# Performance work log

Hardware: AMD Instinct MI355X
Metric: run time of the kernel (lower is better)

## Reference

```python
import jax, jax.numpy as jnp
import numpy as np

B, T, E, H = 2, 2048, 1024, 16
Dh = E // H  # head_size = 64


def setup_inputs() -> dict:
    key = jax.random.key(0)
    ks = jax.random.split(key, 6)
    s = E ** -0.5
    x = jax.random.normal(ks[0], (B, T, E), dtype=jnp.float32)
    Wq = jax.random.normal(ks[1], (H, E, Dh), dtype=jnp.float32) * s
    Wk = jax.random.normal(ks[2], (H, E, Dh), dtype=jnp.float32) * s
    Wv = jax.random.normal(ks[3], (H, E, Dh), dtype=jnp.float32) * s
    wo_w = jax.random.normal(ks[4], (E, E), dtype=jnp.float32) * s  # torch Linear weight [out,in]
    wo_b = jax.random.normal(ks[5], (E,), dtype=jnp.float32) * 0.01
    return {"x": x, "Wq": Wq, "Wk": Wk, "Wv": Wv, "wo_w": wo_w, "wo_b": wo_b}


def reference(x, Wq, Wk, Wv, wo_w, wo_b):
    # Batched equivalent of the per-head Python loop: project all heads at once.
    q = jnp.einsum('bte,hed->bhtd', x, Wq)
    k = jnp.einsum('bte,hed->bhtd', x, Wk)
    v = jnp.einsum('bte,hed->bhtd', x, Wv)
    scale = Dh ** -0.5
    scores = jnp.einsum('bhtd,bhsd->bhts', q, k) * scale  # [B,H,T,T]
    causal = jnp.tril(jnp.ones((T, T), dtype=bool))
    scores = jnp.where(causal, scores, jnp.finfo(scores.dtype).min)
    att = jax.nn.softmax(scores, axis=-1)
    out = jnp.einsum('bhts,bhsd->bhtd', att, v)  # [B,H,T,Dh]
    # concat heads (head order along last dim, matching torch.cat over heads)
    out = out.transpose(0, 2, 1, 3).reshape(B, T, E)
    return out @ wo_w.T + wo_b
```

## Files before the change

### kernel.cpp

```cpp
#include <hip/hip_runtime.h>

#define B_ 2
#define T_ 2048
#define E_ 1024
#define H_ 16
#define DH 64

typedef unsigned short u16;
typedef unsigned int u32;
typedef __bf16 bf16x8 __attribute__((ext_vector_type(8)));
typedef float f32x4 __attribute__((ext_vector_type(4)));

__device__ __forceinline__ u16 f2bf(float f) {
  u32 u = __builtin_bit_cast(u32, f);
  u = u + 0x7FFFu + ((u >> 16) & 1u);
  return (u16)(u >> 16);
}
__device__ __forceinline__ float bf2f(u16 v) {
  return __builtin_bit_cast(float, (u32)v << 16);
}
__device__ __forceinline__ bf16x8 ldfrag(const u16* p) { return *(const bf16x8*)p; }

__device__ __forceinline__ void gload_lds16(const u16* g, u16* l) {
  __builtin_amdgcn_global_load_lds((const __attribute__((address_space(1))) u32*)g,
                                   (__attribute__((address_space(3))) u32*)l, 16, 0, 0);
}
template <int IMM>
__device__ __forceinline__ float swz(float v) {
  return __builtin_bit_cast(float, __builtin_amdgcn_ds_swizzle(__builtin_bit_cast(int, v), IMM));
}

__global__ void k_conv_x(const float* __restrict__ src, u16* __restrict__ dst) {
  u32 i = (blockIdx.x * 256u + threadIdx.x) * 8u;
  float4 a = *(const float4*)(src + i);
  float4 b = *(const float4*)(src + i + 4);
  uint4 v;
  v.x = (u32)f2bf(a.x) | ((u32)f2bf(a.y) << 16);
  v.y = (u32)f2bf(a.z) | ((u32)f2bf(a.w) << 16);
  v.z = (u32)f2bf(b.x) | ((u32)f2bf(b.y) << 16);
  v.w = (u32)f2bf(b.z) | ((u32)f2bf(b.w) << 16);
  *(uint4*)(dst + i) = v;
}

__global__ __launch_bounds__(256) void k_conv_wT(const float* __restrict__ Wq, const float* __restrict__ Wk,
                                                 const float* __restrict__ Wv, u16* __restrict__ wT) {
  __shared__ __align__(16) u16 Ls[64][68];
  const int t = threadIdx.x;
  const int e0 = blockIdx.x * 64;
  const int h = blockIdx.y;
  const int which = blockIdx.z;
  const float* src = (which == 0) ? Wq : ((which == 1) ? Wk : Wv);
  const float scale = (which == 0) ? 0.18033688011112042f : 1.0f;
#pragma unroll
  for (int p = 0; p < 4; p++) {
    int idx = p * 256 + t;
    int row = idx >> 4, ch = idx & 15;
    float4 v = *(const float4*)(src + ((size_t)h * E_ + e0 + row) * DH + ch * 4);
    uint2 pk;
    pk.x = (u32)f2bf(v.x * scale) | ((u32)f2bf(v.y * scale) << 16);
    pk.y = (u32)f2bf(v.z * scale) | ((u32)f2bf(v.w * scale) << 16);
    *(uint2*)(&Ls[row][ch * 4]) = pk;
  }
  __syncthreads();
  u16* dst = wT + ((size_t)which * H_ + h) * (DH * E_);
#pragma unroll
  for (int p = 0; p < 4; p++) {
    int idx = p * 256 + t;
    int d = idx >> 4, ec = idx & 15;
    uint2 pk;
    pk.x = (u32)Ls[ec * 4 + 0][d] | ((u32)Ls[ec * 4 + 1][d] << 16);
    pk.y = (u32)Ls[ec * 4 + 2][d] | ((u32)Ls[ec * 4 + 3][d] << 16);
    *(uint2*)(dst + (size_t)d * E_ + e0 + ec * 4) = pk;
  }
}

__global__ __launch_bounds__(256, 3) void k_qkv(const u16* __restrict__ xb, const u16* __restrict__ wT,
                                                u16* __restrict__ Qb, u16* __restrict__ Kb,
                                                u16* __restrict__ VbT) {
  __shared__ __align__(16) u16 As[128 * 64];
  __shared__ __align__(16) u16 Bs[128 * 64];
  const int tid = threadIdx.x;
  const int w = tid >> 6, lane = tid & 63, quad = lane >> 4, lr = lane & 15;
  const int wr = w >> 1, wc = w & 1;
  const int t0 = blockIdx.x * 128;
  const int n0 = blockIdx.y * 128;
  const int sr = lane >> 3, sc = lane & 7;

  f32x4 acc[4][4];
  const f32x4 z4 = {0.f, 0.f, 0.f, 0.f};
#pragma unroll
  for (int i = 0; i < 4; i++)
#pragma unroll
    for (int j = 0; j < 4; j++) acc[i][j] = z4;

  for (int k0 = 0; k0 < E_; k0 += 64) {
    __syncthreads();
#pragma unroll
    for (int ii = 0; ii < 4; ii++) {
      int ra = w * 32 + ii * 8 + sr;
      gload_lds16(xb + (size_t)(t0 + ra) * E_ + k0 + ((sc ^ (ra & 7)) << 3),
                  As + (w * 32 + ii * 8) * 64);
      gload_lds16(wT + (size_t)(n0 + ra) * E_ + k0 + ((sc ^ (ra & 7)) << 3),
                  Bs + (w * 32 + ii * 8) * 64);
    }
    __syncthreads();
#pragma unroll
    for (int kk = 0; kk < 2; kk++) {
      bf16x8 af[4], bfv[4];
#pragma unroll
      for (int rt = 0; rt < 4; rt++) {
        int row = wr * 64 + rt * 16 + lr;
        af[rt] = ldfrag(As + row * 64 + (((kk * 4 + quad) ^ (row & 7)) << 3));
      }
#pragma unroll
      for (int ct = 0; ct < 4; ct++) {
        int row = wc * 64 + ct * 16 + lr;
        bfv[ct] = ldfrag(Bs + row * 64 + (((kk * 4 + quad) ^ (row & 7)) << 3));
      }
#pragma unroll
      for (int rt = 0; rt < 4; rt++)
#pragma unroll
        for (int ct = 0; ct < 4; ct++)
          acc[rt][ct] = __builtin_amdgcn_mfma_f32_16x16x32_bf16(af[rt], bfv[ct], acc[rt][ct], 0, 0, 0);
    }
  }

  const int qkv = n0 >> 10;
  if (qkv < 2) {
    u16* outp = (qkv == 0) ? Qb : Kb;
#pragma unroll
    for (int rt = 0; rt < 4; rt++)
#pragma unroll
      for (int ct = 0; ct < 4; ct++) {
        int n = n0 + wc * 64 + ct * 16 + lr;
        int h = (n >> 6) & 15, d = n & 63;
#pragma unroll
        for (int r = 0; r < 4; r++) {
          int t = t0 + wr * 64 + rt * 16 + quad * 4 + r;
          int bb = t >> 11, tt = t & 2047;
          outp[(((size_t)bb * H_ + h) * T_ + tt) * DH + d] = f2bf(acc[rt][ct][r]);
        }
      }
  } else {
#pragma unroll
    for (int rt = 0; rt < 4; rt++)
#pragma unroll
      for (int ct = 0; ct < 4; ct++) {
        int n = n0 + wc * 64 + ct * 16 + lr;
        int h = (n >> 6) & 15, d = n & 63;
        int t = t0 + wr * 64 + rt * 16 + quad * 4;
        int bb = t >> 11, tt = t & 2047;
        uint2 pk;
        pk.x = (u32)f2bf(acc[rt][ct][0]) | ((u32)f2bf(acc[rt][ct][1]) << 16);
        pk.y = (u32)f2bf(acc[rt][ct][2]) | ((u32)f2bf(acc[rt][ct][3]) << 16);
        *(uint2*)(VbT + (((size_t)bb * H_ + h) * DH + d) * T_ + tt) = pk;
      }
  }
}

__global__ __launch_bounds__(256, 4) void k_attn(const u16* __restrict__ Qb, const u16* __restrict__ Kb,
                                                 const u16* __restrict__ VbT, u16* __restrict__ O0,
                                                 u16* __restrict__ O1, float* __restrict__ Mb,
                                                 float* __restrict__ Lb) {
  __shared__ __align__(16) u16 Qs[64][72];
  __shared__ __align__(16) u16 Ks[64][72];
  __shared__ __align__(16) u16 Vts[64][72];
  __shared__ __align__(16) u16 Ps[64][72];
  const int tid = threadIdx.x;
  const int w = tid >> 6, lane = tid & 63, quad = lane >> 4, lr = lane & 15;
  const int i = blockIdx.x >> 1, s = blockIdx.x & 1;
  const int h = blockIdx.y, bb = blockIdx.z;
  const u16* qb = Qb + ((size_t)bb * H_ + h) * (size_t)(T_ * DH);
  const u16* kb = Kb + ((size_t)bb * H_ + h) * (size_t)(T_ * DH);
  const u16* vbT = VbT + ((size_t)bb * H_ + h) * (size_t)(T_ * DH);
  const f32x4 z4 = {0.f, 0.f, 0.f, 0.f};

  for (int jb = 0; jb < 2; jb++) {
    const int qt = jb ? i : (31 - i);
    const int sg = jb ? (1 - s) : s;
    const int t0 = qt * 64;
    __syncthreads();
#pragma unroll
    for (int p = 0; p < 2; p++) {
      int lin = p * 256 + tid;
      int r = lin >> 3, c = (lin & 7) * 8;
      *(uint4*)(&Qs[r][c]) = *(const uint4*)(qb + (size_t)(t0 + r) * DH + c);
    }

    f32x4 o_acc[4];
#pragma unroll
    for (int ct = 0; ct < 4; ct++) o_acc[ct] = z4;
    float m_i[4], l_i[4];
#pragma unroll
    for (int r = 0; r < 4; r++) { m_i[r] = -__builtin_inff(); l_i[r] = 0.f; }

    for (int jt = sg; jt <= qt; jt += 2) {
      const int j0 = jt * 64;
      __syncthreads();
#pragma unroll
      for (int p = 0; p < 2; p++) {
        int lin = p * 256 + tid;
        int r = lin >> 3, c = (lin & 7) * 8;
        *(uint4*)(&Ks[r][c]) = *(const uint4*)(kb + (size_t)(j0 + r) * DH + c);
        *(uint4*)(&Vts[r][c]) = *(const uint4*)(vbT + (size_t)r * T_ + j0 + c);
      }
      __syncthreads();

      f32x4 s_acc[4];
#pragma unroll
      for (int ct = 0; ct < 4; ct++) s_acc[ct] = z4;
      bf16x8 aq0 = ldfrag(&Qs[w * 16 + lr][quad * 8]);
      bf16x8 aq1 = ldfrag(&Qs[w * 16 + lr][32 + quad * 8]);
#pragma unroll
      for (int ct = 0; ct < 4; ct++) {
        bf16x8 b0 = ldfrag(&Ks[ct * 16 + lr][quad * 8]);
        bf16x8 b1 = ldfrag(&Ks[ct * 16 + lr][32 + quad * 8]);
        s_acc[ct] = __builtin_amdgcn_mfma_f32_16x16x32_bf16(aq0, b0, s_acc[ct], 0, 0, 0);
        s_acc[ct] = __builtin_amdgcn_mfma_f32_16x16x32_bf16(aq1, b1, s_acc[ct], 0, 0, 0);
      }

      if (jt == qt) {
        int trow = w * 16 + quad * 4;
#pragma unroll
        for (int ct = 0; ct < 4; ct++) {
          int sc = ct * 16 + lr;
#pragma unroll
          for (int r = 0; r < 4; r++)
            if (sc > trow + r) s_acc[ct][r] = -__builtin_inff();
        }
      }

      float alpha[4], rsum[4];
#pragma unroll
      for (int r = 0; r < 4; r++) {
        float v = fmaxf(fmaxf(s_acc[0][r], s_acc[1][r]), fmaxf(s_acc[2][r], s_acc[3][r]));
        v = fmaxf(v, swz<0x041F>(v));
        v = fmaxf(v, swz<0x081F>(v));
        v = fmaxf(v, swz<0x101F>(v));
        v = fmaxf(v, swz<0x201F>(v));
        float mnew = fmaxf(m_i[r], v);
        alpha[r] = __builtin_amdgcn_exp2f(m_i[r] - mnew);
        m_i[r] = mnew;
        rsum[r] = 0.f;
      }
#pragma unroll
      for (int ct = 0; ct < 4; ct++)
#pragma unroll
        for (int r = 0; r < 4; r++) {
          float p = __builtin_amdgcn_exp2f(s_acc[ct][r] - m_i[r]);
          rsum[r] += p;
          Ps[w * 16 + quad * 4 + r][ct * 16 + lr] = (u16)(__builtin_bit_cast(u32, p) >> 16);
        }
#pragma unroll
      for (int r = 0; r < 4; r++) {
        float v = rsum[r];
        v += swz<0x041F>(v);
        v += swz<0x081F>(v);
        v += swz<0x101F>(v);
        v += swz<0x201F>(v);
        l_i[r] = l_i[r] * alpha[r] + v;
      }
#pragma unroll
      for (int ct = 0; ct < 4; ct++)
#pragma unroll
        for (int r = 0; r < 4; r++) o_acc[ct][r] *= alpha[r];

      bf16x8 ap0 = ldfrag(&Ps[w * 16 + lr][quad * 8]);
      bf16x8 ap1 = ldfrag(&Ps[w * 16 + lr][32 + quad * 8]);
#pragma unroll
      for (int ct = 0; ct < 4; ct++) {
        bf16x8 b0 = ldfrag(&Vts[ct * 16 + lr][quad * 8]);
        bf16x8 b1 = ldfrag(&Vts[ct * 16 + lr][32 + quad * 8]);
        o_acc[ct] = __builtin_amdgcn_mfma_f32_16x16x32_bf16(ap0, b0, o_acc[ct], 0, 0, 0);
        o_acc[ct] = __builtin_amdgcn_mfma_f32_16x16x32_bf16(ap1, b1, o_acc[ct], 0, 0, 0);
      }
    }

    u16* op = (sg == 0) ? O0 : O1;
    float inv[4];
#pragma unroll
    for (int r = 0; r < 4; r++) inv[r] = (l_i[r] > 0.f) ? (1.0f / l_i[r]) : 0.f;
#pragma unroll
    for (int ct = 0; ct < 4; ct++)
#pragma unroll
      for (int r = 0; r < 4; r++) {
        int t = t0 + w * 16 + quad * 4 + r;
        op[((size_t)bb * T_ + t) * E_ + h * DH + ct * 16 + lr] = f2bf(o_acc[ct][r] * inv[r]);
      }
    if (lr == 0) {
#pragma unroll
      for (int r = 0; r < 4; r++) {
        int t = t0 + w * 16 + quad * 4 + r;
        int idx = ((sg * B_ + bb) * H_ + h) * T_ + t;
        Mb[idx] = m_i[r];
        Lb[idx] = l_i[r];
      }
    }
  }
}

__global__ void k_combine(u16* __restrict__ AO, const u16* __restrict__ O1,
                          const float* __restrict__ Mb, const float* __restrict__ Lb) {
  int idx = blockIdx.x * 256 + threadIdx.x;
  int e0 = idx * 4;
  int bb = e0 >> 21, t = (e0 >> 10) & 2047, hh = (e0 >> 6) & 15;
  int r0 = (bb * H_ + hh) * T_ + t;
  int r1 = r0 + B_ * H_ * T_;
  float m0 = Mb[r0], l0 = Lb[r0], m1 = Mb[r1], l1 = Lb[r1];
  float m = fmaxf(m0, m1);
  float w0 = l0 * __builtin_amdgcn_exp2f(m0 - m);
  float w1 = l1 * __builtin_amdgcn_exp2f(m1 - m);
  float inv = 1.0f / (w0 + w1);
  float a0 = w0 * inv, a1 = w1 * inv;
  uint2 u0 = *(const uint2*)(AO + e0);
  uint2 u1 = *(const uint2*)(O1 + e0);
  float f0 = a0 * bf2f((u16)u0.x) + a1 * bf2f((u16)u1.x);
  float f1 = a0 * bf2f((u16)(u0.x >> 16)) + a1 * bf2f((u16)(u1.x >> 16));
  float f2 = a0 * bf2f((u16)u0.y) + a1 * bf2f((u16)u1.y);
  float f3 = a0 * bf2f((u16)(u0.y >> 16)) + a1 * bf2f((u16)(u1.y >> 16));
  uint2 o;
  o.x = (u32)f2bf(f0) | ((u32)f2bf(f1) << 16);
  o.y = (u32)f2bf(f2) | ((u32)f2bf(f3) << 16);
  *(uint2*)(AO + e0) = o;
}

__global__ __launch_bounds__(256) void k_oproj(const u16* __restrict__ AO, const u16* __restrict__ woB,
                                               const float* __restrict__ bias, float* __restrict__ out) {
  __shared__ __align__(16) u16 Xs[128][40];
  __shared__ __align__(16) u16 Ws[64][40];
  const int tid = threadIdx.x;
  const int w = tid >> 6, lane = tid & 63, quad = lane >> 4, lr = lane & 15;
  const int r0 = blockIdx.x * 128, n0 = blockIdx.y * 64;
  const u16* xrow = AO + (size_t)r0 * E_;
  const u16* wsrc = woB + (size_t)n0 * E_;

  f32x4 acc[2][4];
  const f32x4 z4 = {0.f, 0.f, 0.f, 0.f};
#pragma unroll
  for (int i = 0; i < 2; i++)
#pragma unroll
    for (int j = 0; j < 4; j++) acc[i][j] = z4;

  for (int e0 = 0; e0 < E_; e0 += 32) {
    __syncthreads();
#pragma unroll
    for (int p = 0; p < 2; p++) {
      int lin = p * 256 + tid;
      int r = lin >> 2, c = (lin & 3) * 8;
      *(uint4*)(&Xs[r][c]) = *(const uint4*)(xrow + (size_t)r * E_ + e0 + c);
    }
    {
      int r = tid >> 2, c = (tid & 3) * 8;
      *(uint4*)(&Ws[r][c]) = *(const uint4*)(wsrc + (size_t)r * E_ + e0 + c);
    }
    __syncthreads();
    bf16x8 af[2], bfr[4];
#pragma unroll
    for (int rt = 0; rt < 2; rt++) af[rt] = ldfrag(&Xs[w * 32 + rt * 16 + lr][quad * 8]);
#pragma unroll
    for (int ct = 0; ct < 4; ct++) bfr[ct] = ldfrag(&Ws[ct * 16 + lr][quad * 8]);
#pragma unroll
    for (int rt = 0; rt < 2; rt++)
#pragma unroll
      for (int ct = 0; ct < 4; ct++)
        acc[rt][ct] = __builtin_amdgcn_mfma_f32_16x16x32_bf16(af[rt], bfr[ct], acc[rt][ct], 0, 0, 0);
  }

#pragma unroll
  for (int ct = 0; ct < 4; ct++) {
    float bv = bias[n0 + ct * 16 + lr];
#pragma unroll
    for (int rt = 0; rt < 2; rt++)
#pragma unroll
      for (int r = 0; r < 4; r++) {
        int row = r0 + w * 32 + rt * 16 + quad * 4 + r;
        out[(size_t)row * E_ + n0 + ct * 16 + lr] = acc[rt][ct][r] + bv;
      }
  }
}

extern "C" void kernel_launch(void* const* d_in, const int* in_sizes, int n_in,
                              void* d_out, int out_size, void* d_ws, size_t ws_size,
                              hipStream_t stream) {
  const float* x = (const float*)d_in[0];
  const float* Wq = (const float*)d_in[1];
  const float* Wk = (const float*)d_in[2];
  const float* Wv = (const float*)d_in[3];
  const float* wo_w = (const float*)d_in[4];
  const float* wo_b = (const float*)d_in[5];
  float* out = (float*)d_out;
  char* ws = (char*)d_ws;

  u16* xb  = (u16*)(ws + 0);
  u16* wT  = (u16*)(ws + 8388608);
  u16* woB = (u16*)(ws + 14680064);
  u16* Qb  = (u16*)(ws + 16777216);
  u16* Kb  = (u16*)(ws + 25165824);
  u16* VbT = (u16*)(ws + 33554432);
  u16* AO  = (u16*)(ws + 41943040);
  u16* O1  = xb;
  float* Mb = (float*)(ws + 8388608);
  float* Lb = (float*)(ws + 8912896);

  k_conv_x<<<2048, 256, 0, stream>>>(x, xb);
  k_conv_wT<<<dim3(16, 16, 3), 256, 0, stream>>>(Wq, Wk, Wv, wT);
  k_conv_x<<<512, 256, 0, stream>>>(wo_w, woB);
  k_qkv<<<dim3(32, 24), 256, 0, stream>>>(xb, wT, Qb, Kb, VbT);
  k_attn<<<dim3(32, 16, 2), 256, 0, stream>>>(Qb, Kb, VbT, AO, O1, Mb, Lb);
  k_combine<<<4096, 256, 0, stream>>>(AO, O1, Mb, Lb);
  k_oproj<<<dim3(32, 16), 256, 0, stream>>>(AO, woB, wo_b, out);
}
```

Baseline: 199.9 us.

## Use XOR-swizzled direct-to-LDS loads and transposed MFMA in attention and out-projection

Attention now loads Q, K and V^T tiles with global_load_lds into an XOR-swizzled unpadded LDS layout. It swaps the MFMA operands so each lane holds one query row, which reduces the softmax reductions to two cross-lane shuffles and lets P be written as packed 8-byte stores. The output projection moves to 128x128 tiles with K=64 steps and a 2x2 wave layout, using the same swizzled direct-to-LDS loads. The aim is fewer LDS bank conflicts, fewer register round trips on loads, and more data reuse per tile, at the risk of higher register pressure and a smaller grid for the out-projection.

```diff
diff --git a/kernel.cpp b/kernel.cpp
--- a/kernel.cpp
+++ b/kernel.cpp
@@ -24,10 +24,6 @@
 __device__ __forceinline__ void gload_lds16(const u16* g, u16* l) {
   __builtin_amdgcn_global_load_lds((const __attribute__((address_space(1))) u32*)g,
                                    (__attribute__((address_space(3))) u32*)l, 16, 0, 0);
-}
-template <int IMM>
-__device__ __forceinline__ float swz(float v) {
-  return __builtin_bit_cast(float, __builtin_amdgcn_ds_swizzle(__builtin_bit_cast(int, v), IMM));
 }
 
 __global__ void k_conv_x(const float* __restrict__ src, u16* __restrict__ dst) {
@@ -162,12 +158,14 @@
                                                  const u16* __restrict__ VbT, u16* __restrict__ O0,
                                                  u16* __restrict__ O1, float* __restrict__ Mb,
                                                  float* __restrict__ Lb) {
-  __shared__ __align__(16) u16 Qs[64][72];
-  __shared__ __align__(16) u16 Ks[64][72];
-  __shared__ __align__(16) u16 Vts[64][72];
-  __shared__ __align__(16) u16 Ps[64][72];
+  __shared__ __align__(16) u16 Qs[64 * 64];
+  __shared__ __align__(16) u16 Ks[64 * 64];
+  __shared__ __align__(16) u16 Vts[64 * 64];
+  __shared__ __align__(16) u16 Ps[64 * 64];
   const int tid = threadIdx.x;
   const int w = tid >> 6, lane = tid & 63, quad = lane >> 4, lr = lane & 15;
+  const int l7 = lr & 7;
+  const int srow = lane >> 3, schunk = lane & 7;
   const int i = blockIdx.x >> 1, s = blockIdx.x & 1;
   const int h = blockIdx.y, bb = blockIdx.z;
   const u16* qb = Qb + ((size_t)bb * H_ + h) * (size_t)(T_ * DH);
@@ -181,120 +179,111 @@
     const int t0 = qt * 64;
     __syncthreads();
 #pragma unroll
-    for (int p = 0; p < 2; p++) {
-      int lin = p * 256 + tid;
-      int r = lin >> 3, c = (lin & 7) * 8;
-      *(uint4*)(&Qs[r][c]) = *(const uint4*)(qb + (size_t)(t0 + r) * DH + c);
+    for (int ii = 0; ii < 2; ii++) {
+      int r = w * 16 + ii * 8 + srow;
+      gload_lds16(qb + (size_t)(t0 + r) * DH + ((schunk ^ (r & 7)) << 3),
+                  Qs + (w * 16 + ii * 8) * 64);
     }
 
     f32x4 o_acc[4];
 #pragma unroll
-    for (int ct = 0; ct < 4; ct++) o_acc[ct] = z4;
-    float m_i[4], l_i[4];
-#pragma unroll
-    for (int r = 0; r < 4; r++) { m_i[r] = -__builtin_inff(); l_i[r] = 0.f; }
+    for (int dt = 0; dt < 4; dt++) o_acc[dt] = z4;
+    float m_i = -__builtin_inff(), l_i = 0.f;
 
     for (int jt = sg; jt <= qt; jt += 2) {
       const int j0 = jt * 64;
       __syncthreads();
 #pragma unroll
-      for (int p = 0; p < 2; p++) {
-        int lin = p * 256 + tid;
-        int r = lin >> 3, c = (lin & 7) * 8;
-        *(uint4*)(&Ks[r][c]) = *(const uint4*)(kb + (size_t)(j0 + r) * DH + c);
-        *(uint4*)(&Vts[r][c]) = *(const uint4*)(vbT + (size_t)r * T_ + j0 + c);
+      for (int ii = 0; ii < 2; ii++) {
+        int r = w * 16 + ii * 8 + srow;
+        gload_lds16(kb + (size_t)(j0 + r) * DH + ((schunk ^ (r & 7)) << 3),
+                    Ks + (w * 16 + ii * 8) * 64);
+        gload_lds16(vbT + (size_t)r * T_ + j0 + ((schunk ^ (r & 7)) << 3),
+                    Vts + (w * 16 + ii * 8) * 64);
       }
       __syncthreads();
 
       f32x4 s_acc[4];
 #pragma unroll
-      for (int ct = 0; ct < 4; ct++) s_acc[ct] = z4;
-      bf16x8 aq0 = ldfrag(&Qs[w * 16 + lr][quad * 8]);
-      bf16x8 aq1 = ldfrag(&Qs[w * 16 + lr][32 + quad * 8]);
-#pragma unroll
-      for (int ct = 0; ct < 4; ct++) {
-        bf16x8 b0 = ldfrag(&Ks[ct * 16 + lr][quad * 8]);
-        bf16x8 b1 = ldfrag(&Ks[ct * 16 + lr][32 + quad * 8]);
-        s_acc[ct] = __builtin_amdgcn_mfma_f32_16x16x32_bf16(aq0, b0, s_acc[ct], 0, 0, 0);
-        s_acc[ct] = __builtin_amdgcn_mfma_f32_16x16x32_bf16(aq1, b1, s_acc[ct], 0, 0, 0);
+      for (int st = 0; st < 4; st++) s_acc[st] = z4;
+#pragma unroll
+      for (int kk = 0; kk < 2; kk++) {
+        bf16x8 bq = ldfrag(Qs + (w * 16 + lr) * 64 + (((kk * 4 + quad) ^ l7) << 3));
+#pragma unroll
+        for (int st = 0; st < 4; st++) {
+          bf16x8 ak = ldfrag(Ks + (st * 16 + lr) * 64 + (((kk * 4 + quad) ^ l7) << 3));
+          s_acc[st] = __builtin_amdgcn_mfma_f32_16x16x32_bf16(ak, bq, s_acc[st], 0, 0, 0);
+        }
       }
 
       if (jt == qt) {
-        int trow = w * 16 + quad * 4;
-#pragma unroll
-        for (int ct = 0; ct < 4; ct++) {
-          int sc = ct * 16 + lr;
+        int qloc = w * 16 + lr;
+#pragma unroll
+        for (int st = 0; st < 4; st++) {
+          int sbase = st * 16 + quad * 4;
 #pragma unroll
           for (int r = 0; r < 4; r++)
-            if (sc > trow + r) s_acc[ct][r] = -__builtin_inff();
+            if (sbase + r > qloc) s_acc[st][r] = -__builtin_inff();
         }
       }
 
-      float alpha[4], rsum[4];
-#pragma unroll
-      for (int r = 0; r < 4; r++) {
-        float v = fmaxf(fmaxf(s_acc[0][r], s_acc[1][r]), fmaxf(s_acc[2][r], s_acc[3][r]));
-        v = fmaxf(v, swz<0x041F>(v));
-        v = fmaxf(v, swz<0x081F>(v));
-        v = fmaxf(v, swz<0x101F>(v));
-        v = fmaxf(v, swz<0x201F>(v));
-        float mnew = fmaxf(m_i[r], v);
-        alpha[r] = __builtin_amdgcn_exp2f(m_i[r] - mnew);
-        m_i[r] = mnew;
-        rsum[r] = 0.f;
-      }
-#pragma unroll
-      for (int ct = 0; ct < 4; ct++)
-#pragma unroll
-        for (int r = 0; r < 4; r++) {
-          float p = __builtin_amdgcn_exp2f(s_acc[ct][r] - m_i[r]);
-          rsum[r] += p;
-          Ps[w * 16 + quad * 4 + r][ct * 16 + lr] = (u16)(__builtin_bit_cast(u32, p) >> 16);
+      float v01 = fmaxf(fmaxf(s_acc[0][0], s_acc[0][1]), fmaxf(s_acc[0][2], s_acc[0][3]));
+      float v23 = fmaxf(fmaxf(s_acc[1][0], s_acc[1][1]), fmaxf(s_acc[1][2], s_acc[1][3]));
+      float v45 = fmaxf(fmaxf(s_acc[2][0], s_acc[2][1]), fmaxf(s_acc[2][2], s_acc[2][3]));
+      float v67 = fmaxf(fmaxf(s_acc[3][0], s_acc[3][1]), fmaxf(s_acc[3][2], s_acc[3][3]));
+      float v = fmaxf(fmaxf(v01, v23), fmaxf(v45, v67));
+      v = fmaxf(v, __shfl_xor(v, 16));
+      v = fmaxf(v, __shfl_xor(v, 32));
+      float mnew = fmaxf(m_i, v);
+      float alpha = __builtin_amdgcn_exp2f(m_i - mnew);
+      m_i = mnew;
+      float rsum = 0.f;
+#pragma unroll
+      for (int st = 0; st < 4; st++) {
+        float p0 = __builtin_amdgcn_exp2f(s_acc[st][0] - m_i);
+        float p1 = __builtin_amdgcn_exp2f(s_acc[st][1] - m_i);
+        float p2 = __builtin_amdgcn_exp2f(s_acc[st][2] - m_i);
+        float p3 = __builtin_amdgcn_exp2f(s_acc[st][3] - m_i);
+        rsum += (p0 + p1) + (p2 + p3);
+        uint2 pk;
+        pk.x = (__builtin_bit_cast(u32, p0) >> 16) | (__builtin_bit_cast(u32, p1) & 0xffff0000u);
+        pk.y = (__builtin_bit_cast(u32, p2) >> 16) | (__builtin_bit_cast(u32, p3) & 0xffff0000u);
+        *(uint2*)(Ps + (w * 16 + lr) * 64 + (((st * 2 + (quad >> 1)) ^ l7) << 3) + ((quad & 1) << 2)) = pk;
+      }
+      rsum += __shfl_xor(rsum, 16);
+      rsum += __shfl_xor(rsum, 32);
+      l_i = l_i * alpha + rsum;
+#pragma unroll
+      for (int dt = 0; dt < 4; dt++)
+#pragma unroll
+        for (int r = 0; r < 4; r++) o_acc[dt][r] *= alpha;
+
+#pragma unroll
+      for (int kk = 0; kk < 2; kk++) {
+        bf16x8 bp = ldfrag(Ps + (w * 16 + lr) * 64 + (((kk * 4 + quad) ^ l7) << 3));
+#pragma unroll
+        for (int dt = 0; dt < 4; dt++) {
+          bf16x8 av = ldfrag(Vts + (dt * 16 + lr) * 64 + (((kk * 4 + quad) ^ l7) << 3));
+          o_acc[dt] = __builtin_amdgcn_mfma_f32_16x16x32_bf16(av, bp, o_acc[dt], 0, 0, 0);
         }
-#pragma unroll
-      for (int r = 0; r < 4; r++) {
-        float v = rsum[r];
-        v += swz<0x041F>(v);
-        v += swz<0x081F>(v);
-        v += swz<0x101F>(v);
-        v += swz<0x201F>(v);
-        l_i[r] = l_i[r] * alpha[r] + v;
-      }
-#pragma unroll
-      for (int ct = 0; ct < 4; ct++)
-#pragma unroll
-        for (int r = 0; r < 4; r++) o_acc[ct][r] *= alpha[r];
-
-      bf16x8 ap0 = ldfrag(&Ps[w * 16 + lr][quad * 8]);
-      bf16x8 ap1 = ldfrag(&Ps[w * 16 + lr][32 + quad * 8]);
-#pragma unroll
-      for (int ct = 0; ct < 4; ct++) {
-        bf16x8 b0 = ldfrag(&Vts[ct * 16 + lr][quad * 8]);
-        bf16x8 b1 = ldfrag(&Vts[ct * 16 + lr][32 + quad * 8]);
-        o_acc[ct] = __builtin_amdgcn_mfma_f32_16x16x32_bf16(ap0, b0, o_acc[ct], 0, 0, 0);
-        o_acc[ct] = __builtin_amdgcn_mfma_f32_16x16x32_bf16(ap1, b1, o_acc[ct], 0, 0, 0);
       }
     }
 
     u16* op = (sg == 0) ? O0 : O1;
-    float inv[4];
-#pragma unroll
-    for (int r = 0; r < 4; r++) inv[r] = (l_i[r] > 0.f) ? (1.0f / l_i[r]) : 0.f;
-#pragma unroll
-    for (int ct = 0; ct < 4; ct++)
-#pragma unroll
-      for (int r = 0; r < 4; r++) {
-        int t = t0 + w * 16 + quad * 4 + r;
-        op[((size_t)bb * T_ + t) * E_ + h * DH + ct * 16 + lr] = f2bf(o_acc[ct][r] * inv[r]);
-      }
-    if (lr == 0) {
-#pragma unroll
-      for (int r = 0; r < 4; r++) {
-        int t = t0 + w * 16 + quad * 4 + r;
-        int idx = ((sg * B_ + bb) * H_ + h) * T_ + t;
-        Mb[idx] = m_i[r];
-        Lb[idx] = l_i[r];
-      }
+    float inv = (l_i > 0.f) ? (1.0f / l_i) : 0.f;
+    int t = t0 + w * 16 + lr;
+    u16* orow = op + ((size_t)bb * T_ + t) * E_ + h * DH;
+#pragma unroll
+    for (int dt = 0; dt < 4; dt++) {
+      uint2 pk;
+      pk.x = (u32)f2bf(o_acc[dt][0] * inv) | ((u32)f2bf(o_acc[dt][1] * inv) << 16);
+      pk.y = (u32)f2bf(o_acc[dt][2] * inv) | ((u32)f2bf(o_acc[dt][3] * inv) << 16);
+      *(uint2*)(orow + dt * 16 + quad * 4) = pk;
+    }
+    if (quad == 0) {
+      int idx = ((sg * B_ + bb) * H_ + h) * T_ + t;
+      Mb[idx] = m_i;
+      Lb[idx] = l_i;
     }
   }
 }
@@ -324,57 +313,64 @@
   *(uint2*)(AO + e0) = o;
 }
 
-__global__ __launch_bounds__(256) void k_oproj(const u16* __restrict__ AO, const u16* __restrict__ woB,
-                                               const float* __restrict__ bias, float* __restrict__ out) {
-  __shared__ __align__(16) u16 Xs[128][40];
-  __shared__ __align__(16) u16 Ws[64][40];
+__global__ __launch_bounds__(256, 3) void k_oproj(const u16* __restrict__ AO, const u16* __restrict__ woB,
+                                                  const float* __restrict__ bias, float* __restrict__ out) {
+  __shared__ __align__(16) u16 As[128 * 64];
+  __shared__ __align__(16) u16 Bs[128 * 64];
   const int tid = threadIdx.x;
   const int w = tid >> 6, lane = tid & 63, quad = lane >> 4, lr = lane & 15;
-  const int r0 = blockIdx.x * 128, n0 = blockIdx.y * 64;
-  const u16* xrow = AO + (size_t)r0 * E_;
-  const u16* wsrc = woB + (size_t)n0 * E_;
-
-  f32x4 acc[2][4];
+  const int wr = w >> 1, wc = w & 1;
+  const int r0 = blockIdx.x * 128, n0 = blockIdx.y * 128;
+  const int sr = lane >> 3, sc = lane & 7;
+
+  f32x4 acc[4][4];
   const f32x4 z4 = {0.f, 0.f, 0.f, 0.f};
 #pragma unroll
-  for (int i = 0; i < 2; i++)
+  for (int i = 0; i < 4; i++)
 #pragma unroll
     for (int j = 0; j < 4; j++) acc[i][j] = z4;
 
-  for (int e0 = 0; e0 < E_; e0 += 32) {
+  for (int k0 = 0; k0 < E_; k0 += 64) {
     __syncthreads();
 #pragma unroll
-    for (int p = 0; p < 2; p++) {
-      int lin = p * 256 + tid;
-      int r = lin >> 2, c = (lin & 3) * 8;
-      *(uint4*)(&Xs[r][c]) = *(const uint4*)(xrow + (size_t)r * E_ + e0 + c);
-    }
-    {
-      int r = tid >> 2, c = (tid & 3) * 8;
-      *(uint4*)(&Ws[r][c]) = *(const uint4*)(wsrc + (size_t)r * E_ + e0 + c);
+    for (int ii = 0; ii < 4; ii++) {
+      int ra = w * 32 + ii * 8 + sr;
+      gload_lds16(AO + (size_t)(r0 + ra) * E_ + k0 + ((sc ^ (ra & 7)) << 3),
+                  As + (w * 32 + ii * 8) * 64);
+      gload_lds16(woB + (size_t)(n0 + ra) * E_ + k0 + ((sc ^ (ra & 7)) << 3),
+                  Bs + (w * 32 + ii * 8) * 64);
     }
     __syncthreads();
-    bf16x8 af[2], bfr[4];
-#pragma unroll
-    for (int rt = 0; rt < 2; rt++) af[rt] = ldfrag(&Xs[w * 32 + rt * 16 + lr][quad * 8]);
-#pragma unroll
-    for (int ct = 0; ct < 4; ct++) bfr[ct] = ldfrag(&Ws[ct * 16 + lr][quad * 8]);
-#pragma unroll
-    for (int rt = 0; rt < 2; rt++)
-#pragma unroll
-      for (int ct = 0; ct < 4; ct++)
-        acc[rt][ct] = __builtin_amdgcn_mfma_f32_16x16x32_bf16(af[rt], bfr[ct], acc[rt][ct], 0, 0, 0);
+#pragma unroll
+    for (int kk = 0; kk < 2; kk++) {
+      bf16x8 af[4], bfv[4];
+#pragma unroll
+      for (int rt = 0; rt < 4; rt++) {
+        int row = wr * 64 + rt * 16 + lr;
+        af[rt] = ldfrag(As + row * 64 + (((kk * 4 + quad) ^ (row & 7)) << 3));
+      }
+#pragma unroll
+      for (int ct = 0; ct < 4; ct++) {
+        int row = wc * 64 + ct * 16 + lr;
+        bfv[ct] = ldfrag(Bs + row * 64 + (((kk * 4 + quad) ^ (row & 7)) << 3));
+      }
+#pragma unroll
+      for (int rt = 0; rt < 4; rt++)
+#pragma unroll
+        for (int ct = 0; ct < 4; ct++)
+          acc[rt][ct] = __builtin_amdgcn_mfma_f32_16x16x32_bf16(af[rt], bfv[ct], acc[rt][ct], 0, 0, 0);
+    }
   }
 
 #pragma unroll
   for (int ct = 0; ct < 4; ct++) {
-    float bv = bias[n0 + ct * 16 + lr];
-#pragma unroll
-    for (int rt = 0; rt < 2; rt++)
+    float bv = bias[n0 + wc * 64 + ct * 16 + lr];
+#pragma unroll
+    for (int rt = 0; rt < 4; rt++)
 #pragma unroll
       for (int r = 0; r < 4; r++) {
-        int row = r0 + w * 32 + rt * 16 + quad * 4 + r;
-        out[(size_t)row * E_ + n0 + ct * 16 + lr] = acc[rt][ct][r] + bv;
+        int row = r0 + wr * 64 + rt * 16 + quad * 4 + r;
+        out[(size_t)row * E_ + n0 + wc * 64 + ct * 16 + lr] = acc[rt][ct][r] + bv;
       }
   }
 }
@@ -408,5 +404,5 @@
   k_qkv<<<dim3(32, 24), 256, 0, stream>>>(xb, wT, Qb, Kb, VbT);
   k_attn<<<dim3(32, 16, 2), 256, 0, stream>>>(Qb, Kb, VbT, AO, O1, Mb, Lb);
   k_combine<<<4096, 256, 0, stream>>>(AO, O1, Mb, Lb);
-  k_oproj<<<dim3(32, 16), 256, 0, stream>>>(AO, woB, wo_b, out);
-}
+  k_oproj<<<dim3(32, 8), 256, 0, stream>>>(AO, woB, wo_b, out);
+}
```

After: 181.2 us. -9.4%, faster.
